# Performance work log

Measured on AMD Instinct MI355X. Metric: run time of the kernel, lower is better.

The kernel has to match this reference:

```python
import jax, jax.numpy as jnp
import numpy as np

K = 6
EPS = 1e-7
BN_EPS = 1e-5


def tagconv(x, row, col, n, lins, bias, mw1, mb1, bng, bnb, mw2, mb2):
    # gcn_norm: symmetric normalization, no self-loops, edge_weight = 1
    deg = jax.ops.segment_sum(jnp.ones(row.shape[0], x.dtype), col, num_segments=n)
    dis = jnp.where(deg > 0, jax.lax.rsqrt(jnp.maximum(deg, 1.0)), 0.0)
    norm = dis[row] * dis[col]  # [E]
    out = x @ lins[0]
    h = x
    for k in range(1, K + 1):
        # message: relu(edge_weight * x_j) + eps, then scatter-add to destination
        msg = jax.nn.relu(norm[:, None] * h[row]) + EPS  # [E, C]
        h = jax.ops.segment_sum(msg, col, num_segments=n)
        out = out + h @ lins[k]
    out = out + bias
    # MLP: Linear -> BatchNorm1d(eval: running mean 0, var 1) -> ReLU -> Dropout(eval) -> Linear
    z = out @ mw1 + mb1
    z = bng * (z * (1.0 / np.sqrt(1.0 + BN_EPS))) + bnb
    z = jax.nn.relu(z)
    return z @ mw2 + mb2


def setup_inputs() -> dict:
    key = jax.random.key(0)
    ks = jax.random.split(key, 8)
    N, E, F, H, C = 50000, 800000, 128, 128, 64
    s = 0.05
    return {
        "x": jax.random.normal(ks[0], (N, F), jnp.float32),
        "edge_index": jax.random.randint(ks[1], (2, E), 0, N, jnp.int64),
        "lins1": jax.random.normal(ks[2], (K + 1, F, H), jnp.float32) * s,
        "bias1": jnp.zeros((H,), jnp.float32),
        "m1w1": jax.random.normal(ks[3], (H, 2 * H), jnp.float32) * s,
        "m1b1": jnp.zeros((2 * H,), jnp.float32),
        "bn1g": jnp.ones((2 * H,), jnp.float32),
        "bn1b": jnp.zeros((2 * H,), jnp.float32),
        "m1w2": jax.random.normal(ks[4], (2 * H, H), jnp.float32) * s,
        "m1b2": jnp.zeros((H,), jnp.float32),
        "lins2": jax.random.normal(ks[5], (K + 1, H, C), jnp.float32) * s,
        "bias2": jnp.zeros((C,), jnp.float32),
        "m2w1": jax.random.normal(ks[6], (C, 2 * C), jnp.float32) * s,
        "m2b1": jnp.zeros((2 * C,), jnp.float32),
        "bn2g": jnp.ones((2 * C,), jnp.float32),
        "bn2b": jnp.zeros((2 * C,), jnp.float32),
        "m2w2": jax.random.normal(ks[7], (2 * C, C), jnp.float32) * s,
        "m2b2": jnp.zeros((C,), jnp.float32),
    }


def reference(x, edge_index, lins1, bias1, m1w1, m1b1, bn1g, bn1b, m1w2, m1b2,
              lins2, bias2, m2w1, m2b1, bn2g, bn2b, m2w2, m2b2):
    n = x.shape[0]
    row, col = edge_index[0], edge_index[1]
    h = tagconv(x, row, col, n, lins1, bias1, m1w1, m1b1, bn1g, bn1b, m1w2, m1b2)
    h = jax.nn.relu(h)  # dropout is identity in eval mode
    return tagconv(h, row, col, n, lins2, bias2, m2w1, m2b1, bn2g, bn2b, m2w2, m2b2)
```

## Files before the change

kernel.cpp:

```cpp
#include <hip/hip_runtime.h>
#include <hip/hip_bf16.h>


#define EPS_MSG 1e-7f
#define BNSCALE 0.9999950000374997f
#define LO_INV 0.0009765625f

typedef _Float16 half_t;
typedef _Float16 f16x8 __attribute__((ext_vector_type(8)));
typedef float f32x4 __attribute__((ext_vector_type(4)));

__device__ __forceinline__ void gld16(const char* g, char* l) {
    __builtin_amdgcn_global_load_lds(
        (const __attribute__((address_space(1))) void*)g,
        (__attribute__((address_space(3))) void*)l, 16, 0, 0);
}

__device__ __forceinline__ float hlo(unsigned p) {
    unsigned short u = (unsigned short)(p & 0xffffu);
    half_t h;
    __builtin_memcpy(&h, &u, 2);
    return (float)h;
}
__device__ __forceinline__ float hhi(unsigned p) {
    unsigned short u = (unsigned short)(p >> 16);
    half_t h;
    __builtin_memcpy(&h, &u, 2);
    return (float)h;
}
__device__ __forceinline__ unsigned fpack2(float x, float y) {
    half_t a = (half_t)x, b = (half_t)y;
    unsigned short ua, ub;
    __builtin_memcpy(&ua, &a, 2);
    __builtin_memcpy(&ub, &b, 2);
    return (unsigned)ua | ((unsigned)ub << 16);
}


__global__ void zero_i32(int* __restrict__ p, int n) {
    int i = blockIdx.x * blockDim.x + threadIdx.x;
    if (i < n) p[i] = 0;
}

__global__ void count_deg(const int* __restrict__ col, int* __restrict__ deg, int E) {
    int e = blockIdx.x * blockDim.x + threadIdx.x;
    if (e < E) atomicAdd(&deg[col[e]], 1);
}

__global__ void compute_dis_s(const int* __restrict__ deg, float* __restrict__ dis,
                              float* __restrict__ s, float* __restrict__ rs, int N) {
    int v = blockIdx.x * blockDim.x + threadIdx.x;
    if (v >= N) return;
    int d = deg[v];
    float di = (d > 0) ? rsqrtf((float)d) : 0.f;
    dis[v] = di;
    s[v] = (d > 0) ? di : 1.f;
    rs[v] = (d > 0) ? sqrtf((float)d) : 1.f;
}

__global__ void scan_blk(const int* __restrict__ deg, int* __restrict__ off,
                         int* __restrict__ bsum, int N) {
    __shared__ int sm[1024];
    int i = blockIdx.x * 1024 + threadIdx.x;
    sm[threadIdx.x] = (i < N) ? deg[i] : 0;
    __syncthreads();
    for (int ofs = 1; ofs < 1024; ofs <<= 1) {
        int t = (threadIdx.x >= (unsigned)ofs) ? sm[threadIdx.x - ofs] : 0;
        __syncthreads();
        sm[threadIdx.x] += t;
        __syncthreads();
    }
    if (i < N) off[i + 1] = sm[threadIdx.x];
    if (threadIdx.x == 0) bsum[blockIdx.x] = sm[1023];
}

__global__ void scan_top(int* __restrict__ bsum, int nb) {
    if (threadIdx.x == 0 && blockIdx.x == 0) {
        int a = 0;
        for (int b = 0; b < nb; ++b) {
            int t = bsum[b];
            bsum[b] = a;
            a += t;
        }
    }
}

__global__ void scan_add(int* __restrict__ off, const int* __restrict__ bsum, int N) {
    int i = blockIdx.x * 1024 + threadIdx.x;
    if (i < N) off[i + 1] += bsum[blockIdx.x];
    if (i == 0) off[0] = 0;
}

__global__ void fill_edges(const int* __restrict__ row, const int* __restrict__ col,
                           const int* __restrict__ off, int* __restrict__ cur,
                           unsigned short* __restrict__ esrc, int E) {
    int e = blockIdx.x * blockDim.x + threadIdx.x;
    if (e >= E) return;
    int c = col[e];
    int pos = off[c] + atomicAdd(&cur[c], 1);
    esrc[pos] = (unsigned short)row[e];
}


__global__ void conv_xg(const float* __restrict__ x, half_t* __restrict__ slab,
                        half_t* __restrict__ g0, const float* __restrict__ dis,
                        const float* __restrict__ s, int total) {
    int i = blockIdx.x * blockDim.x + threadIdx.x;
    if (i >= total) return;
    int v = i >> 7, c = i & 127;
    float xv = x[i];
    slab[(size_t)v * 896 + c] = (half_t)(s[v] * xv);
    g0[i] = (half_t)(dis[v] * fmaxf(xv, 0.f));
}

__device__ __forceinline__ void wcv(const float* __restrict__ in, half_t* __restrict__ oh,
                                    half_t* __restrict__ ol, int nm, int K, int Nn, int i) {
    int KT = nm * K;
    int n = i / KT;
    int rem = i - n * KT;
    int km = rem / K, k = rem - km * K;
    float w = in[(size_t)km * K * Nn + (size_t)k * Nn + n];
    half_t h = (half_t)w;
    oh[i] = h;
    ol[i] = (half_t)((w - (float)h) * 1024.f);
}

__global__ void conv_all(const float* l1, const float* l2, const float* a1, const float* b1,
                         const float* a2, const float* b2, half_t* W1h, half_t* W1l,
                         half_t* W2h, half_t* W2l, half_t* M1ah, half_t* M1al, half_t* M1bh,
                         half_t* M1bl, half_t* M2ah, half_t* M2al, half_t* M2bh,
                         half_t* M2bl) {
    int i = blockIdx.x * blockDim.x + threadIdx.x;
    if (i < 114688) {
        wcv(l1, W1h, W1l, 7, 128, 128, i);
    } else if (i < 172032) {
        wcv(l2, W2h, W2l, 7, 128, 64, i - 114688);
    } else if (i < 204800) {
        wcv(a1, M1ah, M1al, 1, 128, 256, i - 172032);
    } else if (i < 237568) {
        wcv(b1, M1bh, M1bl, 1, 256, 128, i - 204800);
    } else if (i < 245760) {
        wcv(a2, M2ah, M2al, 1, 64, 128, i - 237568);
    } else if (i < 253952) {
        wcv(b2, M2bh, M2bl, 1, 128, 64, i - 245760);
    }
}


__global__ void __launch_bounds__(256) prop(const unsigned* __restrict__ gin, int idl,
                                            unsigned* __restrict__ gout, int odl,
                                            const float* __restrict__ dis,
                                            const int* __restrict__ off,
                                            const unsigned short* __restrict__ esrc, int N) {
    const int lane = threadIdx.x & 63;
    const int w = threadIdx.x >> 6;
    const int stride = gridDim.x * 4;
    for (int v = blockIdx.x * 4 + w; v < N; v += stride) {
        int s = off[v], e = off[v + 1];
        float2 A0 = {0.f, 0.f}, A1 = {0.f, 0.f}, A2 = {0.f, 0.f}, A3 = {0.f, 0.f};
        float2 A4 = {0.f, 0.f}, A5 = {0.f, 0.f}, A6 = {0.f, 0.f}, A7 = {0.f, 0.f};
        for (int i = s; i < e; i += 8) {
            unsigned p[8];
            int ok[8];
#pragma unroll
            for (int j = 0; j < 8; ++j) {
                int ij = i + j;
                ok[j] = ij < e;
                int idx = ok[j] ? ij : e - 1;
                p[j] = gin[esrc[idx] * idl + lane];
            }
            A0.x += ok[0] ? hlo(p[0]) : 0.f; A0.y += ok[0] ? hhi(p[0]) : 0.f;
            A1.x += ok[1] ? hlo(p[1]) : 0.f; A1.y += ok[1] ? hhi(p[1]) : 0.f;
            A2.x += ok[2] ? hlo(p[2]) : 0.f; A2.y += ok[2] ? hhi(p[2]) : 0.f;
            A3.x += ok[3] ? hlo(p[3]) : 0.f; A3.y += ok[3] ? hhi(p[3]) : 0.f;
            A4.x += ok[4] ? hlo(p[4]) : 0.f; A4.y += ok[4] ? hhi(p[4]) : 0.f;
            A5.x += ok[5] ? hlo(p[5]) : 0.f; A5.y += ok[5] ? hhi(p[5]) : 0.f;
            A6.x += ok[6] ? hlo(p[6]) : 0.f; A6.y += ok[6] ? hhi(p[6]) : 0.f;
            A7.x += ok[7] ? hlo(p[7]) : 0.f; A7.y += ok[7] ? hhi(p[7]) : 0.f;
        }
        float ax = ((A0.x + A1.x) + (A2.x + A3.x)) + ((A4.x + A5.x) + (A6.x + A7.x));
        float ay = ((A0.y + A1.y) + (A2.y + A3.y)) + ((A4.y + A5.y) + (A6.y + A7.y));
        float dv = dis[v];
        float ce = (float)(e - s) * EPS_MSG;
        float hx = fmaf(dv, ax, ce);
        float hy = fmaf(dv, ay, ce);
        gout[v * odl + lane] = fpack2(dv * hx, dv * hy);
    }
}


template <int BN, int OUTF32>
__global__ __launch_bounds__(256) void gemm(
    int M, int kiters, const half_t* __restrict__ A, int lda,
    const half_t* __restrict__ Bhp, const half_t* __restrict__ Blp, int ldb,
    void* __restrict__ Cp, int ldc, const float* __restrict__ rs, int epi,
    const float* __restrict__ bias, const float* __restrict__ bng,
    const float* __restrict__ bnb, half_t* __restrict__ goutP, int ldp,
    const float* __restrict__ sArr, half_t* __restrict__ goutG, int ldg,
    const float* __restrict__ disArr) {
    constexpr int BM = 64, BK = 64;
    constexpr int WC = (BN == 128) ? 2 : 1;
    constexpr int WROWS = BM / (4 / WC);
    constexpr int MF = WROWS / 16;
    constexpr int NF = 4;
    constexpr int ABY = BM * BK * 2;
    constexpr int BBY = BN * BK * 2;
    constexpr int BUFBY = ABY + 2 * BBY;
    constexpr int ACW = (ABY / 1024) / 4;
    constexpr int BCW = (BBY / 1024) / 4;

    __shared__ char lds[2][BUFBY];

    const int tid = threadIdx.x;
    const int lane = tid & 63;
    const int w = tid >> 6;
    const int wr = w / WC, wc = w % WC;
    const int m0 = blockIdx.x * BM;
    const int n0 = blockIdx.y * BN;
    const int l15 = lane & 15, lq = lane >> 4;
    const int lr8 = lane >> 3, lc8 = lane & 7;

    const char* gA = (const char*)A;
    const char* gBh = (const char*)Bhp;
    const char* gBl = (const char*)Blp;
    const size_t ldaB = (size_t)lda * 2, ldbB = (size_t)ldb * 2;

    auto stage = [&](int kt, int buf) {
        const int k0b = kt * BK * 2;
        char* base = lds[0] + buf * BUFBY;
#pragma unroll
        for (int i = 0; i < ACW; ++i) {
            int c = w * ACW + i;
            int r = c * 8 + lr8;
            int gv = m0 + r;
            if (gv >= M) gv = M - 1;
            int sc = (lc8 ^ (r & 7)) << 4;
            gld16(gA + (size_t)gv * ldaB + k0b + sc, base + c * 1024);
        }
#pragma unroll
        for (int i = 0; i < BCW; ++i) {
            int c = w * BCW + i;
            int r = c * 8 + lr8;
            int sc = (lc8 ^ (r & 7)) << 4;
            size_t goff = (size_t)(n0 + r) * ldbB + k0b + sc;
            gld16(gBh + goff, base + ABY + c * 1024);
            gld16(gBl + goff, base + ABY + BBY + c * 1024);
        }
    };

    f32x4 acch[MF][NF], accl[MF][NF];
#pragma unroll
    for (int fm = 0; fm < MF; ++fm)
#pragma unroll
        for (int fn = 0; fn < NF; ++fn) {
            acch[fm][fn] = (f32x4){0.f, 0.f, 0.f, 0.f};
            accl[fm][fn] = (f32x4){0.f, 0.f, 0.f, 0.f};
        }

    auto compute = [&](int buf) {
        const char* Ab = lds[0] + buf * BUFBY;
        const char* Bhb = Ab + ABY;
        const char* Blb = Ab + ABY + BBY;
#pragma unroll
        for (int ks = 0; ks < 2; ++ks) {
            const int cc = ks * 4 + lq;
            f16x8 af[MF];
#pragma unroll
            for (int fm = 0; fm < MF; ++fm) {
                int r = wr * WROWS + fm * 16 + l15;
                af[fm] = *(const f16x8*)(Ab + r * 128 + ((cc ^ (r & 7)) << 4));
            }
#pragma unroll
            for (int fn = 0; fn < NF; ++fn) {
                int r = wc * 64 + fn * 16 + l15;
                int o = r * 128 + ((cc ^ (r & 7)) << 4);
                f16x8 bhv = *(const f16x8*)(Bhb + o);
                f16x8 blv = *(const f16x8*)(Blb + o);
#pragma unroll
                for (int fm = 0; fm < MF; ++fm) {
                    acch[fm][fn] =
                        __builtin_amdgcn_mfma_f32_16x16x32_f16(af[fm], bhv, acch[fm][fn], 0, 0, 0);
                    accl[fm][fn] =
                        __builtin_amdgcn_mfma_f32_16x16x32_f16(af[fm], blv, accl[fm][fn], 0, 0, 0);
                }
            }
        }
    };

    stage(0, 0);
    int buf = 0;
    for (int kt = 0; kt < kiters; ++kt) {
        __syncthreads();
        if (kt + 1 < kiters) stage(kt + 1, buf ^ 1);
        compute(buf);
        buf ^= 1;
    }

#pragma unroll
    for (int fm = 0; fm < MF; ++fm)
#pragma unroll
        for (int fn = 0; fn < NF; ++fn)
#pragma unroll
            for (int i = 0; i < 4; ++i) {
                int gr = m0 + wr * WROWS + fm * 16 + (lane >> 4) * 4 + i;
                if (gr >= M) continue;
                int gc = n0 + wc * 64 + fn * 16 + (lane & 15);
                float v = acch[fm][fn][i] + accl[fm][fn][i] * LO_INV;
                if (rs) v *= rs[gr];
                if (epi == 1) {
                    v += bias[gc];
                } else if (epi == 2) {
                    v = bng[gc] * ((v + bias[gc]) * BNSCALE) + bnb[gc];
                    v = fmaxf(v, 0.f);
                } else if (epi == 3) {
                    v = fmaxf(v + bias[gc], 0.f);
                }
                if (Cp) {
                    if (OUTF32)
                        ((float*)Cp)[(size_t)gr * ldc + gc] = v;
                    else
                        ((half_t*)Cp)[(size_t)gr * ldc + gc] = (half_t)v;
                }
                if (goutP) goutP[(size_t)gr * ldp + gc] = (half_t)(sArr[gr] * v);
                if (goutG) goutG[(size_t)gr * ldg + gc] = (half_t)(disArr[gr] * v);
            }
}

extern "C" void kernel_launch(void* const* d_in, const int* in_sizes, int n_in,
                              void* d_out, int out_size, void* d_ws, size_t ws_size,
                              hipStream_t stream) {
    const float* x     = (const float*)d_in[0];
    const int*   ei    = (const int*)d_in[1];
    const float* lins1 = (const float*)d_in[2];
    const float* bias1 = (const float*)d_in[3];
    const float* m1w1  = (const float*)d_in[4];
    const float* m1b1  = (const float*)d_in[5];
    const float* bn1g  = (const float*)d_in[6];
    const float* bn1b  = (const float*)d_in[7];
    const float* m1w2  = (const float*)d_in[8];
    const float* m1b2  = (const float*)d_in[9];
    const float* lins2 = (const float*)d_in[10];
    const float* bias2 = (const float*)d_in[11];
    const float* m2w1  = (const float*)d_in[12];
    const float* m2b1  = (const float*)d_in[13];
    const float* bn2g  = (const float*)d_in[14];
    const float* bn2b  = (const float*)d_in[15];
    const float* m2w2  = (const float*)d_in[16];
    const float* m2b2  = (const float*)d_in[17];
    float* out = (float*)d_out;

    const int N = in_sizes[0] / 128;
    const int E = in_sizes[1] / 2;
    const int* row = ei;
    const int* col = ei + E;

    char* ws = (char*)d_ws;
    size_t o = 0;
    auto alloc = [&](size_t bytes) {
        void* p = ws + o;
        o += (bytes + 255) & ~(size_t)255;
        return p;
    };
    int*            deg  = (int*)alloc((size_t)N * 4);
    int*            cur  = (int*)alloc((size_t)N * 4);
    float*          dis  = (float*)alloc((size_t)N * 4);
    float*          sA   = (float*)alloc((size_t)N * 4);
    float*          rsA  = (float*)alloc((size_t)N * 4);
    int*            off  = (int*)alloc((size_t)(N + 1) * 4);
    int*            bsum = (int*)alloc(1024 * 4);
    unsigned short* esrc = (unsigned short*)alloc((size_t)E * 2);
    half_t* g0    = (half_t*)alloc((size_t)N * 128 * 2);
    half_t* ACC   = (half_t*)alloc((size_t)N * 128 * 2);
    half_t* Z     = (half_t*)alloc((size_t)N * 256 * 2);
    half_t* ACC2  = (half_t*)alloc((size_t)N * 64 * 2);
    half_t* Wc1h  = (half_t*)alloc((size_t)128 * 896 * 2);
    half_t* Wc1l  = (half_t*)alloc((size_t)128 * 896 * 2);
    half_t* Wc2h  = (half_t*)alloc((size_t)64 * 896 * 2);
    half_t* Wc2l  = (half_t*)alloc((size_t)64 * 896 * 2);
    half_t* Wm1ah = (half_t*)alloc((size_t)256 * 128 * 2);
    half_t* Wm1al = (half_t*)alloc((size_t)256 * 128 * 2);
    half_t* Wm1bh = (half_t*)alloc((size_t)128 * 256 * 2);
    half_t* Wm1bl = (half_t*)alloc((size_t)128 * 256 * 2);
    half_t* Wm2ah = (half_t*)alloc((size_t)128 * 64 * 2);
    half_t* Wm2al = (half_t*)alloc((size_t)128 * 64 * 2);
    half_t* Wm2bh = (half_t*)alloc((size_t)64 * 128 * 2);
    half_t* Wm2bl = (half_t*)alloc((size_t)64 * 128 * 2);
    half_t* slab  = (half_t*)alloc((size_t)N * 896 * 2);
    (void)ws_size;

    const int TPB = 256;
    const int nb = (N + 1023) / 1024;
    zero_i32<<<(N + TPB - 1) / TPB, TPB, 0, stream>>>(deg, N);
    zero_i32<<<(N + TPB - 1) / TPB, TPB, 0, stream>>>(cur, N);
    count_deg<<<(E + TPB - 1) / TPB, TPB, 0, stream>>>(col, deg, E);
    compute_dis_s<<<(N + TPB - 1) / TPB, TPB, 0, stream>>>(deg, dis, sA, rsA, N);
    scan_blk<<<nb, 1024, 0, stream>>>(deg, off, bsum, N);
    scan_top<<<1, 64, 0, stream>>>(bsum, nb);
    scan_add<<<nb, 1024, 0, stream>>>(off, bsum, N);
    fill_edges<<<(E + TPB - 1) / TPB, TPB, 0, stream>>>(row, col, off, cur, esrc, E);
    conv_all<<<(253952 + TPB - 1) / TPB, TPB, 0, stream>>>(
        lins1, lins2, m1w1, m1w2, m2w1, m2w2, Wc1h, Wc1l, Wc2h, Wc2l, Wm1ah, Wm1al, Wm1bh,
        Wm1bl, Wm2ah, Wm2al, Wm2bh, Wm2bl);
    conv_xg<<<(N * 128 + TPB - 1) / TPB, TPB, 0, stream>>>(x, slab, g0, dis, sA, N * 128);

    unsigned* slabU = (unsigned*)slab;
    unsigned* g0U = (unsigned*)g0;
    const int HG = (N + 63) / 64;
    auto launch_prop = [&](const unsigned* gi, int idl, unsigned* go, int odl) {
        prop<<<2048, 256, 0, stream>>>(gi, idl, go, odl, dis, off, esrc, N);
    };

    launch_prop(g0U, 64, slabU + 64, 448);
    for (int k = 2; k <= 6; ++k)
        launch_prop(slabU + (size_t)(k - 1) * 64, 448, slabU + (size_t)k * 64, 448);
    gemm<128, 0><<<dim3(HG, 1), 256, 0, stream>>>(
        N, 14, slab, 896, Wc1h, Wc1l, 896, ACC, 128, rsA, 1, bias1, nullptr, nullptr, nullptr, 0,
        nullptr, nullptr, 0, nullptr);
    gemm<128, 0><<<dim3(HG, 2), 256, 0, stream>>>(
        N, 2, ACC, 128, Wm1ah, Wm1al, 128, Z, 256, nullptr, 2, m1b1, bn1g, bn1b, nullptr, 0,
        nullptr, nullptr, 0, nullptr);
    gemm<128, 0><<<dim3(HG, 1), 256, 0, stream>>>(
        N, 4, Z, 256, Wm1bh, Wm1bl, 256, nullptr, 0, nullptr, 3, m1b2, nullptr, nullptr, slab,
        896, sA, g0, 128, dis);

    launch_prop(g0U, 64, slabU + 64, 448);
    for (int k = 2; k <= 6; ++k)
        launch_prop(slabU + (size_t)(k - 1) * 64, 448, slabU + (size_t)k * 64, 448);
    gemm<64, 0><<<dim3(HG, 1), 256, 0, stream>>>(
        N, 14, slab, 896, Wc2h, Wc2l, 896, ACC2, 64, rsA, 1, bias2, nullptr, nullptr, nullptr, 0,
        nullptr, nullptr, 0, nullptr);
    gemm<128, 0><<<dim3(HG, 1), 256, 0, stream>>>(
        N, 1, ACC2, 64, Wm2ah, Wm2al, 64, Z, 128, nullptr, 2, m2b1, bn2g, bn2b, nullptr, 0,
        nullptr, nullptr, 0, nullptr);
    gemm<64, 1><<<dim3(HG, 1), 256, 0, stream>>>(
        N, 2, Z, 128, Wm2bh, Wm2bl, 128, out, 64, nullptr, 1, m2b2, nullptr, nullptr, nullptr, 0,
        nullptr, nullptr, 0, nullptr);
}
```

Before: 752.6 us.

## Project layer-2 features to 64 channels before propagation using Horner-style recursion

For the second TAGConv layer, the hidden features are first multiplied by all seven 128x64 weight matrices, and propagation then runs as a Horner recursion on 64-channel data instead of propagating 128-channel features six times. The constant EPS message term is carried forward through precomputed column sums of the weights. Each edge gather now reads half as many channels. The cost is an extra projection GEMM up front and a reordering of the fp16 rounding, which could shift accuracy.

```diff
diff --git a/kernel.cpp b/kernel.cpp
--- a/kernel.cpp
+++ b/kernel.cpp
@@ -134,7 +134,13 @@
     if (i < 114688) {
         wcv(l1, W1h, W1l, 7, 128, 128, i);
     } else if (i < 172032) {
-        wcv(l2, W2h, W2l, 7, 128, 64, i - 114688);
+        int j = i - 114688;
+        int np = j >> 7, k = j & 127;
+        int km = np >> 6, n = np & 63;
+        float w = l2[(size_t)km * 128 * 64 + (size_t)k * 64 + n];
+        half_t h = (half_t)w;
+        W2h[j] = h;
+        W2l[j] = (half_t)((w - (float)h) * 1024.f);
     } else if (i < 204800) {
         wcv(a1, M1ah, M1al, 1, 128, 256, i - 172032);
     } else if (i < 237568) {
@@ -144,6 +150,16 @@
     } else if (i < 253952) {
         wcv(b2, M2bh, M2bl, 1, 128, 64, i - 245760);
     }
+}
+
+__global__ void conv_trows(const float* __restrict__ l2, float* __restrict__ T) {
+    int j = threadIdx.x >> 6;
+    int c = threadIdx.x & 63;
+    if (j >= 6) return;
+    float a = 0.f;
+    for (int k = j + 1; k <= 6; ++k)
+        for (int kk = 0; kk < 128; ++kk) a += l2[(size_t)k * 128 * 64 + kk * 64 + c];
+    T[j * 64 + c] = a;
 }
 
 
@@ -189,15 +205,57 @@
 }
 
 
+template <int FINAL>
+__global__ void __launch_bounds__(256) prop64(
+    const half_t* __restrict__ uin, int ldu, const half_t* __restrict__ pj, int ldp,
+    half_t* __restrict__ uout, int ldo, const float* __restrict__ dis,
+    const int* __restrict__ off, const unsigned short* __restrict__ esrc,
+    const float* __restrict__ tj, const float* __restrict__ bias2, int N) {
+    const int c = threadIdx.x & 63;
+    const int w = threadIdx.x >> 6;
+    const int stride = gridDim.x * 4;
+    for (int v = blockIdx.x * 4 + w; v < N; v += stride) {
+        int s = off[v], e = off[v + 1];
+        float a0 = 0.f, a1 = 0.f, a2 = 0.f, a3 = 0.f;
+        float a4 = 0.f, a5 = 0.f, a6 = 0.f, a7 = 0.f;
+        for (int i = s; i < e; i += 8) {
+            float q[8];
+            int ok[8];
+#pragma unroll
+            for (int j = 0; j < 8; ++j) {
+                int ij = i + j;
+                ok[j] = ij < e;
+                int idx = ok[j] ? ij : e - 1;
+                q[j] = (float)uin[(size_t)esrc[idx] * ldu + c];
+            }
+            a0 += ok[0] ? q[0] : 0.f;
+            a1 += ok[1] ? q[1] : 0.f;
+            a2 += ok[2] ? q[2] : 0.f;
+            a3 += ok[3] ? q[3] : 0.f;
+            a4 += ok[4] ? q[4] : 0.f;
+            a5 += ok[5] ? q[5] : 0.f;
+            a6 += ok[6] ? q[6] : 0.f;
+            a7 += ok[7] ? q[7] : 0.f;
+        }
+        float acc = ((a0 + a1) + (a2 + a3)) + ((a4 + a5) + (a6 + a7));
+        float dv = dis[v];
+        float base = (float)pj[(size_t)v * ldp + c] + (float)(e - s) * EPS_MSG * tj[c];
+        float u = fmaf(dv, acc, base);
+        if (FINAL)
+            uout[(size_t)v * ldo + c] = (half_t)(u + bias2[c]);
+        else
+            uout[(size_t)v * ldo + c] = (half_t)(dv * u);
+    }
+}
+
+
 template <int BN, int OUTF32>
 __global__ __launch_bounds__(256) void gemm(
     int M, int kiters, const half_t* __restrict__ A, int lda,
-    const half_t* __restrict__ Bhp, const half_t* __restrict__ Blp, int ldb,
+    const half_t* __restrict__ Bhp, const half_t* __restrict__ Blp, int ldb, int noff,
     void* __restrict__ Cp, int ldc, const float* __restrict__ rs, int epi,
     const float* __restrict__ bias, const float* __restrict__ bng,
-    const float* __restrict__ bnb, half_t* __restrict__ goutP, int ldp,
-    const float* __restrict__ sArr, half_t* __restrict__ goutG, int ldg,
-    const float* __restrict__ disArr) {
+    const float* __restrict__ bnb) {
     constexpr int BM = 64, BK = 64;
     constexpr int WC = (BN == 128) ? 2 : 1;
     constexpr int WROWS = BM / (4 / WC);
@@ -216,7 +274,7 @@
     const int w = tid >> 6;
     const int wr = w / WC, wc = w % WC;
     const int m0 = blockIdx.x * BM;
-    const int n0 = blockIdx.y * BN;
+    const int n0 = blockIdx.y * BN + noff;
     const int l15 = lane & 15, lq = lane >> 4;
     const int lr8 = lane >> 3, lc8 = lane & 7;
 
@@ -315,14 +373,10 @@
                 } else if (epi == 3) {
                     v = fmaxf(v + bias[gc], 0.f);
                 }
-                if (Cp) {
-                    if (OUTF32)
-                        ((float*)Cp)[(size_t)gr * ldc + gc] = v;
-                    else
-                        ((half_t*)Cp)[(size_t)gr * ldc + gc] = (half_t)v;
-                }
-                if (goutP) goutP[(size_t)gr * ldp + gc] = (half_t)(sArr[gr] * v);
-                if (goutG) goutG[(size_t)gr * ldg + gc] = (half_t)(disArr[gr] * v);
+                if (OUTF32)
+                    ((float*)Cp)[(size_t)gr * ldc + gc] = v;
+                else
+                    ((half_t*)Cp)[(size_t)gr * ldc + gc] = (half_t)v;
             }
 }
 
@@ -368,15 +422,17 @@
     float*          rsA  = (float*)alloc((size_t)N * 4);
     int*            off  = (int*)alloc((size_t)(N + 1) * 4);
     int*            bsum = (int*)alloc(1024 * 4);
+    float*          Trow = (float*)alloc(6 * 64 * 4);
     unsigned short* esrc = (unsigned short*)alloc((size_t)E * 2);
     half_t* g0    = (half_t*)alloc((size_t)N * 128 * 2);
     half_t* ACC   = (half_t*)alloc((size_t)N * 128 * 2);
     half_t* Z     = (half_t*)alloc((size_t)N * 256 * 2);
+    half_t* H1    = (half_t*)alloc((size_t)N * 128 * 2);
     half_t* ACC2  = (half_t*)alloc((size_t)N * 64 * 2);
     half_t* Wc1h  = (half_t*)alloc((size_t)128 * 896 * 2);
     half_t* Wc1l  = (half_t*)alloc((size_t)128 * 896 * 2);
-    half_t* Wc2h  = (half_t*)alloc((size_t)64 * 896 * 2);
-    half_t* Wc2l  = (half_t*)alloc((size_t)64 * 896 * 2);
+    half_t* Wc2h  = (half_t*)alloc((size_t)448 * 128 * 2);
+    half_t* Wc2l  = (half_t*)alloc((size_t)448 * 128 * 2);
     half_t* Wm1ah = (half_t*)alloc((size_t)256 * 128 * 2);
     half_t* Wm1al = (half_t*)alloc((size_t)256 * 128 * 2);
     half_t* Wm1bh = (half_t*)alloc((size_t)128 * 256 * 2);
@@ -401,38 +457,46 @@
     conv_all<<<(253952 + TPB - 1) / TPB, TPB, 0, stream>>>(
         lins1, lins2, m1w1, m1w2, m2w1, m2w2, Wc1h, Wc1l, Wc2h, Wc2l, Wm1ah, Wm1al, Wm1bh,
         Wm1bl, Wm2ah, Wm2al, Wm2bh, Wm2bl);
+    conv_trows<<<1, 384, 0, stream>>>(lins2, Trow);
     conv_xg<<<(N * 128 + TPB - 1) / TPB, TPB, 0, stream>>>(x, slab, g0, dis, sA, N * 128);
 
     unsigned* slabU = (unsigned*)slab;
     unsigned* g0U = (unsigned*)g0;
     const int HG = (N + 63) / 64;
-    auto launch_prop = [&](const unsigned* gi, int idl, unsigned* go, int odl) {
-        prop<<<2048, 256, 0, stream>>>(gi, idl, go, odl, dis, off, esrc, N);
-    };
-
-    launch_prop(g0U, 64, slabU + 64, 448);
+
+    prop<<<2048, 256, 0, stream>>>(g0U, 64, slabU + 64, 448, dis, off, esrc, N);
     for (int k = 2; k <= 6; ++k)
-        launch_prop(slabU + (size_t)(k - 1) * 64, 448, slabU + (size_t)k * 64, 448);
+        prop<<<2048, 256, 0, stream>>>(slabU + (size_t)(k - 1) * 64, 448,
+                                       slabU + (size_t)k * 64, 448, dis, off, esrc, N);
     gemm<128, 0><<<dim3(HG, 1), 256, 0, stream>>>(
-        N, 14, slab, 896, Wc1h, Wc1l, 896, ACC, 128, rsA, 1, bias1, nullptr, nullptr, nullptr, 0,
-        nullptr, nullptr, 0, nullptr);
+        N, 14, slab, 896, Wc1h, Wc1l, 896, 0, ACC, 128, rsA, 1, bias1, nullptr, nullptr);
     gemm<128, 0><<<dim3(HG, 2), 256, 0, stream>>>(
-        N, 2, ACC, 128, Wm1ah, Wm1al, 128, Z, 256, nullptr, 2, m1b1, bn1g, bn1b, nullptr, 0,
-        nullptr, nullptr, 0, nullptr);
+        N, 2, ACC, 128, Wm1ah, Wm1al, 128, 0, Z, 256, nullptr, 2, m1b1, bn1g, bn1b);
     gemm<128, 0><<<dim3(HG, 1), 256, 0, stream>>>(
-        N, 4, Z, 256, Wm1bh, Wm1bl, 256, nullptr, 0, nullptr, 3, m1b2, nullptr, nullptr, slab,
-        896, sA, g0, 128, dis);
-
-    launch_prop(g0U, 64, slabU + 64, 448);
-    for (int k = 2; k <= 6; ++k)
-        launch_prop(slabU + (size_t)(k - 1) * 64, 448, slabU + (size_t)k * 64, 448);
+        N, 4, Z, 256, Wm1bh, Wm1bl, 256, 0, H1, 128, nullptr, 3, m1b2, nullptr, nullptr);
+
+    gemm<64, 0><<<dim3(HG, 6), 256, 0, stream>>>(
+        N, 2, H1, 128, Wc2h, Wc2l, 128, 0, slab, 448, nullptr, 0, nullptr, nullptr, nullptr);
     gemm<64, 0><<<dim3(HG, 1), 256, 0, stream>>>(
-        N, 14, slab, 896, Wc2h, Wc2l, 896, ACC2, 64, rsA, 1, bias2, nullptr, nullptr, nullptr, 0,
-        nullptr, nullptr, 0, nullptr);
+        N, 2, H1, 128, Wc2h, Wc2l, 128, 384, slab, 448, dis, 0, nullptr, nullptr, nullptr);
+
+    half_t* ub0 = g0;
+    half_t* ub1 = g0 + (size_t)N * 64;
+    prop64<0><<<2048, 256, 0, stream>>>(slab + 384, 448, slab + 320, 448, ub0, 64, dis, off,
+                                        esrc, Trow + 5 * 64, nullptr, N);
+    prop64<0><<<2048, 256, 0, stream>>>(ub0, 64, slab + 256, 448, ub1, 64, dis, off, esrc,
+                                        Trow + 4 * 64, nullptr, N);
+    prop64<0><<<2048, 256, 0, stream>>>(ub1, 64, slab + 192, 448, ub0, 64, dis, off, esrc,
+                                        Trow + 3 * 64, nullptr, N);
+    prop64<0><<<2048, 256, 0, stream>>>(ub0, 64, slab + 128, 448, ub1, 64, dis, off, esrc,
+                                        Trow + 2 * 64, nullptr, N);
+    prop64<0><<<2048, 256, 0, stream>>>(ub1, 64, slab + 64, 448, ub0, 64, dis, off, esrc,
+                                        Trow + 1 * 64, nullptr, N);
+    prop64<1><<<2048, 256, 0, stream>>>(ub0, 64, slab, 448, ACC2, 64, dis, off, esrc,
+                                        Trow + 0 * 64, bias2, N);
+
     gemm<128, 0><<<dim3(HG, 1), 256, 0, stream>>>(
-        N, 1, ACC2, 64, Wm2ah, Wm2al, 64, Z, 128, nullptr, 2, m2b1, bn2g, bn2b, nullptr, 0,
-        nullptr, nullptr, 0, nullptr);
+        N, 1, ACC2, 64, Wm2ah, Wm2al, 64, 0, Z, 128, nullptr, 2, m2b1, bn2g, bn2b);
     gemm<64, 1><<<dim3(HG, 1), 256, 0, stream>>>(
-        N, 2, Z, 128, Wm2bh, Wm2bl, 128, out, 64, nullptr, 1, m2b2, nullptr, nullptr, nullptr, 0,
-        nullptr, nullptr, 0, nullptr);
-}
+        N, 2, Z, 128, Wm2bh, Wm2bl, 128, 0, out, 64, nullptr, 1, m2b2, nullptr, nullptr);
+}
```

Result: faster. 713.0 us (-5.3%).
